# Kernel optimization log

Measured on AMD Instinct MI355X. Metric: run time of the kernel, lower is better.

The kernel has to match this reference:

```python
import jax, jax.numpy as jnp
import numpy as np

C_Z = 128
C_HID = 128

def setup_inputs() -> dict:
    key = jax.random.key(0)
    ks = jax.random.split(key, 8)
    B, N = 1, 512
    z = jax.random.normal(ks[0], (B, N, N, C_Z), dtype=jnp.float32)
    mask = jnp.ones((B, N, N), dtype=jnp.float32)
    s = 0.02
    params = {
        'ln_w': jnp.ones((C_Z,), jnp.float32),
        'ln_b': jnp.zeros((C_Z,), jnp.float32),
        'W_ap': jax.random.normal(ks[1], (C_Z, C_HID), jnp.float32) * s,
        'b_ap': jnp.zeros((C_HID,), jnp.float32),
        'W_ag': jax.random.normal(ks[2], (C_Z, C_HID), jnp.float32) * s,
        'b_ag': jnp.zeros((C_HID,), jnp.float32),
        'W_bp': jax.random.normal(ks[3], (C_Z, C_HID), jnp.float32) * s,
        'b_bp': jnp.zeros((C_HID,), jnp.float32),
        'W_bg': jax.random.normal(ks[4], (C_Z, C_HID), jnp.float32) * s,
        'b_bg': jnp.zeros((C_HID,), jnp.float32),
        'W_z': jax.random.normal(ks[5], (C_HID, C_Z), jnp.float32) * s,
        'b_z': jnp.zeros((C_Z,), jnp.float32),
    }
    return {'z': z, 'mask': mask, **params}

def _layer_norm(x, w, b, eps=1e-5):
    mu = jnp.mean(x, axis=-1, keepdims=True)
    var = jnp.mean(jnp.square(x - mu), axis=-1, keepdims=True)
    return (x - mu) * jax.lax.rsqrt(var + eps) * w + b

def reference(z, mask, ln_w, ln_b, W_ap, b_ap, W_ag, b_ag, W_bp, b_bp, W_bg, b_bg, W_z, b_z):
    # z: [B, N, N, c_z], mask: [B, N, N]
    z_norm = _layer_norm(z, ln_w, ln_b)
    m = mask[..., None]  # [B, N, N, 1]
    a = (z_norm @ W_ap + b_ap) * jax.nn.sigmoid(z_norm @ W_ag + b_ag) * m
    b = (z_norm @ W_bp + b_bp) * jax.nn.sigmoid(z_norm @ W_bg + b_bg) * m
    # outgoing triangle update: per-channel batched matmul over k
    out = jnp.einsum('bikc,bkjc->bijc', a, b)
    return z + (out @ W_z + b_z)
```

## Files before the change

kernel.cpp:

```cpp
#include <hip/hip_runtime.h>
#include <hip/hip_bf16.h>
#include <cstdint>

#define NN   512
#define CZ   128
#define PTOT (NN * NN)

typedef unsigned short u16;
typedef unsigned int   u32;

using f32x4  = __attribute__((ext_vector_type(4))) float;
using bf16x8 = __attribute__((ext_vector_type(8))) __bf16;

__device__ __forceinline__ u16 f2bf(float x) {
    u32 u = __float_as_uint(x);
    u = (u + 0x7fffu + ((u >> 16) & 1u)) >> 16;
    return (u16)u;
}

__device__ __forceinline__ f32x4 mfma16(bf16x8 a, bf16x8 b, f32x4 c) {
    return __builtin_amdgcn_mfma_f32_16x16x32_bf16(a, b, c, 0, 0, 0);
}

#define GLDS16(src, dst) __builtin_amdgcn_global_load_lds(                  \
        (__attribute__((address_space(1))) void*)(src),                     \
        (__attribute__((address_space(3))) void*)(dst), 16, 0, 0)

__global__ __launch_bounds__(256) void prep_w(
    const float* __restrict__ w0, const float* __restrict__ w1,
    const float* __restrict__ w2, const float* __restrict__ w3,
    const float* __restrict__ w4, u16* __restrict__ out)
{
    const float* srcs[5] = {w0, w1, w2, w3, w4};
    const float* src = srcs[blockIdx.x];
    u16* dst = out + blockIdx.x * 16384;
    for (int idx = threadIdx.x; idx < 16384; idx += 256) {
        int n = idx >> 7, k = idx & 127;
        dst[idx] = f2bf(src[k * 128 + n]);
    }
}

__global__ __launch_bounds__(256) void ln_k(
    const float* __restrict__ z, const float* __restrict__ lnw,
    const float* __restrict__ lnb, u16* __restrict__ zn)
{
    const int t = threadIdx.x;
    const int r = t >> 2, q = t & 3;
    const long prow = (long)blockIdx.x * 64 + r;
    const float4* zp = (const float4*)(z + prow * CZ + q * 32);

    float v[32];
    float s = 0.f, s2 = 0.f;
#pragma unroll
    for (int j = 0; j < 8; ++j) {
        float4 x = zp[j];
        v[j * 4 + 0] = x.x; v[j * 4 + 1] = x.y;
        v[j * 4 + 2] = x.z; v[j * 4 + 3] = x.w;
        s  += x.x + x.y + x.z + x.w;
        s2 += x.x * x.x + x.y * x.y + x.z * x.z + x.w * x.w;
    }
    s  += __shfl_xor(s, 1);  s  += __shfl_xor(s, 2);
    s2 += __shfl_xor(s2, 1); s2 += __shfl_xor(s2, 2);
    float mu  = s * (1.f / 128.f);
    float var = s2 * (1.f / 128.f) - mu * mu;
    float rs  = rsqrtf(var + 1e-5f);

    const float4* lwp = (const float4*)(lnw + q * 32);
    const float4* lbp = (const float4*)(lnb + q * 32);
    u32 pk[16];
#pragma unroll
    for (int j = 0; j < 8; ++j) {
        float4 lw = lwp[j], lb = lbp[j];
        float a0 = (v[j * 4 + 0] - mu) * rs * lw.x + lb.x;
        float a1 = (v[j * 4 + 1] - mu) * rs * lw.y + lb.y;
        float a2 = (v[j * 4 + 2] - mu) * rs * lw.z + lb.z;
        float a3 = (v[j * 4 + 3] - mu) * rs * lw.w + lb.w;
        pk[j * 2 + 0] = (u32)f2bf(a0) | ((u32)f2bf(a1) << 16);
        pk[j * 2 + 1] = (u32)f2bf(a2) | ((u32)f2bf(a3) << 16);
    }
    uint4* dst = (uint4*)(zn + prow * CZ + q * 32);
#pragma unroll
    for (int j = 0; j < 4; ++j) {
        uint4 w4; w4.x = pk[j*4]; w4.y = pk[j*4+1]; w4.z = pk[j*4+2]; w4.w = pk[j*4+3];
        dst[j] = w4;
    }
}

__global__ __launch_bounds__(256) void proj_k(
    const u16* __restrict__ zn,   const float* __restrict__ mask,
    const u16* __restrict__ Wt,
    const float* __restrict__ b_ap, const float* __restrict__ b_ag,
    const float* __restrict__ b_bp, const float* __restrict__ b_bg,
    u16* __restrict__ Aout, u16* __restrict__ Bout)
{
    __shared__ u16  znl[64 * 128];
    __shared__ u16  tbuf[128 * 72];
    __shared__ float lmask[64];

    const int t    = threadIdx.x, l = t & 63, w = t >> 6;
    const int tile = blockIdx.x;
    const int flav = blockIdx.y;
    const int ir   = tile >> 3;
    const int k0   = (tile & 7) << 6;

    {
        const int u = l & 15;
#pragma unroll
        for (int i = 0; i < 4; ++i) {
            int row = (w << 4) + (i << 2) + (l >> 4);
            long prow = flav ? ((long)(k0 + row) * NN + ir)
                             : ((long)ir * NN + k0 + row);
            const u16* src = zn + prow * CZ + ((u ^ (row & 15)) << 3);
            GLDS16(src, &znl[((w << 4) + (i << 2)) << 7]);
        }
    }
    if (t < 64) {
        long prow = flav ? ((long)(k0 + t) * NN + ir) : ((long)ir * NN + k0 + t);
        lmask[t] = mask[prow];
    }
    __syncthreads();

    const u16* Wp = Wt + (flav * 2 + 0) * 16384;
    const u16* Wg = Wt + (flav * 2 + 1) * 16384;

    f32x4 zero4 = {0.f, 0.f, 0.f, 0.f};
    f32x4 accP[4][2], accG[4][2];
#pragma unroll
    for (int mf = 0; mf < 4; ++mf)
#pragma unroll
        for (int nf = 0; nf < 2; ++nf) { accP[mf][nf] = zero4; accG[mf][nf] = zero4; }

#pragma unroll
    for (int kk = 0; kk < 4; ++kk) {
        bf16x8 af[4];
#pragma unroll
        for (int mf = 0; mf < 4; ++mf) {
            int row = (mf << 4) + (l & 15);
            int su  = (kk * 4 + (l >> 4)) ^ (row & 15);
            af[mf] = *(const bf16x8*)&znl[(row << 7) + (su << 3)];
        }
#pragma unroll
        for (int nf = 0; nf < 2; ++nf) {
            int n  = (w << 5) + (nf << 4) + (l & 15);
            int ko = (kk << 5) + ((l >> 4) << 3);
            bf16x8 bp = *(const bf16x8*)&Wp[(n << 7) + ko];
            bf16x8 bg = *(const bf16x8*)&Wg[(n << 7) + ko];
#pragma unroll
            for (int mf = 0; mf < 4; ++mf) {
                accP[mf][nf] = mfma16(af[mf], bp, accP[mf][nf]);
                accG[mf][nf] = mfma16(af[mf], bg, accG[mf][nf]);
            }
        }
    }

    const float* bPp = flav ? b_bp : b_ap;
    const float* bGp = flav ? b_bg : b_ag;
#pragma unroll
    for (int nf = 0; nf < 2; ++nf) {
        int col = (w << 5) + (nf << 4) + (l & 15);
        float bp = bPp[col], bg = bGp[col];
#pragma unroll
        for (int mf = 0; mf < 4; ++mf) {
            int row0 = (mf << 4) + ((l >> 4) << 2);
            float av[4];
#pragma unroll
            for (int rg = 0; rg < 4; ++rg) {
                float pv = accP[mf][nf][rg] + bp;
                float gv = accG[mf][nf][rg] + bg;
                av[rg] = pv * (1.f / (1.f + __expf(-gv))) * lmask[row0 + rg];
            }
            uint2 packed;
            packed.x = (u32)f2bf(av[0]) | ((u32)f2bf(av[1]) << 16);
            packed.y = (u32)f2bf(av[2]) | ((u32)f2bf(av[3]) << 16);
            *(uint2*)&tbuf[col * 72 + row0] = packed;
        }
    }
    __syncthreads();

    u16* outp = flav ? Bout : Aout;
    const int c = t >> 1, half = t & 1;
    u16* dst = outp + (size_t)c * PTOT + (size_t)ir * NN + k0 + half * 32;
    const u16* srcb = &tbuf[c * 72 + half * 32];
#pragma unroll
    for (int e = 0; e < 4; ++e)
        *(uint4*)(dst + e * 8) = *(const uint4*)(srcb + e * 8);
}

__global__ __launch_bounds__(256) void cgemm(
    const u16* __restrict__ A, const u16* __restrict__ B, u16* __restrict__ O)
{
    __shared__ u16 ldsA[2][128 * 64];
    __shared__ u16 ldsB[2][128 * 64];

    const int t = threadIdx.x, l = t & 63, w = t >> 6;
    const int bx0 = blockIdx.x;
    const int bx  = (bx0 & 7) * 256 + (bx0 >> 3);
    const int c  = bx >> 4, ti = (bx >> 2) & 3, tj = bx & 3;
    const u16* Ab = A + (size_t)c * PTOT + (size_t)(ti * 128) * NN;
    const u16* Bb = B + (size_t)c * PTOT + (size_t)(tj * 128) * NN;

    const int lr8 = (w << 3) + (l >> 3);
    const int uu  = l & 7;

    auto stage = [&](int buf, int kt) {
#pragma unroll
        for (int ri = 0; ri < 4; ++ri) {
            int row = ri * 32 + lr8;
            const u16* sa = Ab + (size_t)row * NN + (kt << 6) + ((uu ^ (row & 7)) << 3);
            const u16* sb = Bb + (size_t)row * NN + (kt << 6) + ((uu ^ (row & 7)) << 3);
            u16* da = &ldsA[buf][(ri * 32 + (w << 3)) << 6];
            u16* db = &ldsB[buf][(ri * 32 + (w << 3)) << 6];
            GLDS16(sa, da);
            GLDS16(sb, db);
        }
    };

    const int wm = w >> 1, wn = w & 1;
    f32x4 zero4 = {0.f, 0.f, 0.f, 0.f};
    f32x4 acc[4][4];
#pragma unroll
    for (int mf = 0; mf < 4; ++mf)
#pragma unroll
        for (int nf = 0; nf < 4; ++nf) acc[mf][nf] = zero4;

    stage(0, 0);
    __syncthreads();
    int cur = 0;
    for (int kt = 0; kt < 8; ++kt) {
        if (kt < 7) stage(cur ^ 1, kt + 1);
        const u16* lA = ldsA[cur];
        const u16* lB = ldsB[cur];
#pragma unroll
        for (int kk = 0; kk < 2; ++kk) {
            bf16x8 af[4], bfr[4];
#pragma unroll
            for (int mf = 0; mf < 4; ++mf) {
                int row = (wm << 6) + (mf << 4) + (l & 15);
                int su  = ((kk << 2) + (l >> 4)) ^ (row & 7);
                af[mf] = *(const bf16x8*)&lA[(row << 6) + (su << 3)];
            }
#pragma unroll
            for (int nf = 0; nf < 4; ++nf) {
                int row = (wn << 6) + (nf << 4) + (l & 15);
                int su  = ((kk << 2) + (l >> 4)) ^ (row & 7);
                bfr[nf] = *(const bf16x8*)&lB[(row << 6) + (su << 3)];
            }
#pragma unroll
            for (int mf = 0; mf < 4; ++mf)
#pragma unroll
                for (int nf = 0; nf < 4; ++nf)
                    acc[mf][nf] = mfma16(af[mf], bfr[nf], acc[mf][nf]);
        }
        if (kt < 7) __syncthreads();
        cur ^= 1;
    }

    u16* Ob = O + (size_t)c * PTOT;
    const int i0 = ti * 128 + (wm << 6);
    const int j0 = tj * 128 + (wn << 6);
#pragma unroll
    for (int mf = 0; mf < 4; ++mf)
#pragma unroll
        for (int nf = 0; nf < 4; ++nf) {
            int jc = j0 + (nf << 4) + (l & 15);
#pragma unroll
            for (int rg = 0; rg < 4; ++rg) {
                int irow = i0 + (mf << 4) + ((l >> 4) << 2) + rg;
                Ob[(size_t)irow * NN + jc] = f2bf(acc[mf][nf][rg]);
            }
        }
}

__global__ __launch_bounds__(256) void finalk(
    const u16* __restrict__ O, const u16* __restrict__ Wzt,
    const float* __restrict__ z, const float* __restrict__ bz,
    float* __restrict__ out)
{
    __shared__ u16 Ot[128 * 128];

    const int t = threadIdx.x, l = t & 63, w = t >> 6;
    const int p0 = blockIdx.x << 7;

#pragma unroll
    for (int rep = 0; rep < 8; ++rep) {
        int chunk = rep * 256 + t;
        int c  = chunk >> 4;
        int pc = chunk & 15;
        uint4 vv = *(const uint4*)(O + (size_t)c * PTOT + p0 + (pc << 3));
        const u16* vs = (const u16*)&vv;
#pragma unroll
        for (int e = 0; e < 8; ++e) {
            int p  = (pc << 3) + e;
            int su = (c >> 3) ^ ((p >> 3) & 15) ^ (p & 7);
            Ot[(p << 7) + (su << 3) + (c & 7)] = vs[e];
        }
    }
    __syncthreads();

    f32x4 zero4 = {0.f, 0.f, 0.f, 0.f};
    f32x4 acc[2][8];
#pragma unroll
    for (int mf = 0; mf < 2; ++mf)
#pragma unroll
        for (int nf = 0; nf < 8; ++nf) acc[mf][nf] = zero4;

#pragma unroll
    for (int kk = 0; kk < 4; ++kk) {
        bf16x8 af[2];
#pragma unroll
        for (int mf = 0; mf < 2; ++mf) {
            int p  = (w << 5) + (mf << 4) + (l & 15);
            int su = ((kk << 2) + (l >> 4)) ^ ((p >> 3) & 15) ^ (p & 7);
            af[mf] = *(const bf16x8*)&Ot[(p << 7) + (su << 3)];
        }
#pragma unroll
        for (int nf = 0; nf < 8; ++nf) {
            int co = (nf << 4) + (l & 15);
            bf16x8 bw = *(const bf16x8*)&Wzt[(co << 7) + (kk << 5) + ((l >> 4) << 3)];
#pragma unroll
            for (int mf = 0; mf < 2; ++mf)
                acc[mf][nf] = mfma16(af[mf], bw, acc[mf][nf]);
        }
    }

#pragma unroll
    for (int nf = 0; nf < 8; ++nf) {
        int co = (nf << 4) + (l & 15);
        float b = bz[co];
#pragma unroll
        for (int mf = 0; mf < 2; ++mf) {
#pragma unroll
            for (int rg = 0; rg < 4; ++rg) {
                int p = (w << 5) + (mf << 4) + ((l >> 4) << 2) + rg;
                size_t idx = (size_t)(p0 + p) * CZ + co;
                out[idx] = z[idx] + acc[mf][nf][rg] + b;
            }
        }
    }
}

extern "C" void kernel_launch(void* const* d_in, const int* in_sizes, int n_in,
                              void* d_out, int out_size, void* d_ws, size_t ws_size,
                              hipStream_t stream)
{
    const float* z    = (const float*)d_in[0];
    const float* mask = (const float*)d_in[1];
    const float* lnw  = (const float*)d_in[2];
    const float* lnb  = (const float*)d_in[3];
    const float* Wap  = (const float*)d_in[4];
    const float* bap  = (const float*)d_in[5];
    const float* Wag  = (const float*)d_in[6];
    const float* bag  = (const float*)d_in[7];
    const float* Wbp  = (const float*)d_in[8];
    const float* bbp  = (const float*)d_in[9];
    const float* Wbg  = (const float*)d_in[10];
    const float* bbg  = (const float*)d_in[11];
    const float* Wz   = (const float*)d_in[12];
    const float* bz   = (const float*)d_in[13];
    float* out = (float*)d_out;

    u16* A_t  = (u16*)d_ws;
    u16* B_tt = A_t  + (size_t)CZ * PTOT;
    u16* O_t  = B_tt + (size_t)CZ * PTOT;
    u16* Wt   = O_t  + (size_t)CZ * PTOT;
    u16* Wzt  = Wt + 4 * 16384;
    u16* zn   = O_t;

    prep_w<<<5, 256, 0, stream>>>(Wap, Wag, Wbp, Wbg, Wz, Wt);
    ln_k<<<4096, 256, 0, stream>>>(z, lnw, lnb, zn);
    proj_k<<<dim3(4096, 2), 256, 0, stream>>>(zn, mask, Wt,
                                              bap, bag, bbp, bbg, A_t, B_tt);
    cgemm<<<2048, 256, 0, stream>>>(A_t, B_tt, O_t);
    finalk<<<2048, 256, 0, stream>>>(O_t, Wzt, z, bz, out);
}
```

Measured before the change: 600.9 us.

## Vectorize finalk transpose into LDS and swap MFMA operands for float4 epilogue

The final projection kernel now loads eight channel rows per thread and packs them into 16-byte LDS stores with a new swizzle, replacing scalar 2-byte LDS writes. The MFMA operands are swapped so the weights form the A operand and positions the B operand. Each lane then holds four consecutive output channels, so the residual read of z and the output write become float4 accesses instead of scalar ones. This targets LDS store count and uncoalesced global traffic in the epilogue, at the cost of more registers for the eight held loads.

```diff
diff --git a/kernel.cpp b/kernel.cpp
--- a/kernel.cpp
+++ b/kernel.cpp
@@ -281,60 +281,74 @@
     const int t = threadIdx.x, l = t & 63, w = t >> 6;
     const int p0 = blockIdx.x << 7;
 
-#pragma unroll
-    for (int rep = 0; rep < 8; ++rep) {
-        int chunk = rep * 256 + t;
-        int c  = chunk >> 4;
-        int pc = chunk & 15;
-        uint4 vv = *(const uint4*)(O + (size_t)c * PTOT + p0 + (pc << 3));
-        const u16* vs = (const u16*)&vv;
+    {
+        const int po = t & 15;
+        const int uc = t >> 4;
+        uint4 q[8];
+#pragma unroll
+        for (int cc = 0; cc < 8; ++cc)
+            q[cc] = *(const uint4*)(O + (size_t)(uc * 8 + cc) * PTOT + p0 + po * 8);
 #pragma unroll
         for (int e = 0; e < 8; ++e) {
-            int p  = (pc << 3) + e;
-            int su = (c >> 3) ^ ((p >> 3) & 15) ^ (p & 7);
-            Ot[(p << 7) + (su << 3) + (c & 7)] = vs[e];
+            const int sh = (e & 1) * 16;
+            const int wd = e >> 1;
+            u32 h[8];
+#pragma unroll
+            for (int cc = 0; cc < 8; ++cc)
+                h[cc] = (((const u32*)&q[cc])[wd] >> sh) & 0xffffu;
+            uint4 o;
+            o.x = h[0] | (h[1] << 16);
+            o.y = h[2] | (h[3] << 16);
+            o.z = h[4] | (h[5] << 16);
+            o.w = h[6] | (h[7] << 16);
+            int p  = po * 8 + e;
+            int su = uc ^ (p & 15) ^ ((p >> 4) & 7);
+            *(uint4*)&Ot[(p << 7) + (su << 3)] = o;
         }
     }
     __syncthreads();
 
     f32x4 zero4 = {0.f, 0.f, 0.f, 0.f};
-    f32x4 acc[2][8];
-#pragma unroll
-    for (int mf = 0; mf < 2; ++mf)
-#pragma unroll
-        for (int nf = 0; nf < 8; ++nf) acc[mf][nf] = zero4;
+    f32x4 acc[8][2];
+#pragma unroll
+    for (int m = 0; m < 8; ++m)
+#pragma unroll
+        for (int np = 0; np < 2; ++np) acc[m][np] = zero4;
 
 #pragma unroll
     for (int kk = 0; kk < 4; ++kk) {
-        bf16x8 af[2];
-#pragma unroll
-        for (int mf = 0; mf < 2; ++mf) {
-            int p  = (w << 5) + (mf << 4) + (l & 15);
-            int su = ((kk << 2) + (l >> 4)) ^ ((p >> 3) & 15) ^ (p & 7);
-            af[mf] = *(const bf16x8*)&Ot[(p << 7) + (su << 3)];
-        }
-#pragma unroll
-        for (int nf = 0; nf < 8; ++nf) {
-            int co = (nf << 4) + (l & 15);
-            bf16x8 bw = *(const bf16x8*)&Wzt[(co << 7) + (kk << 5) + ((l >> 4) << 3)];
-#pragma unroll
-            for (int mf = 0; mf < 2; ++mf)
-                acc[mf][nf] = mfma16(af[mf], bw, acc[mf][nf]);
-        }
-    }
-
-#pragma unroll
-    for (int nf = 0; nf < 8; ++nf) {
-        int co = (nf << 4) + (l & 15);
-        float b = bz[co];
-#pragma unroll
-        for (int mf = 0; mf < 2; ++mf) {
-#pragma unroll
-            for (int rg = 0; rg < 4; ++rg) {
-                int p = (w << 5) + (mf << 4) + ((l >> 4) << 2) + rg;
-                size_t idx = (size_t)(p0 + p) * CZ + co;
-                out[idx] = z[idx] + acc[mf][nf][rg] + b;
-            }
+        bf16x8 af[8];
+#pragma unroll
+        for (int m = 0; m < 8; ++m) {
+            int co = (m << 4) + (l & 15);
+            af[m] = *(const bf16x8*)&Wzt[(co << 7) + (kk << 5) + ((l >> 4) << 3)];
+        }
+#pragma unroll
+        for (int np = 0; np < 2; ++np) {
+            int p  = (w << 5) + (np << 4) + (l & 15);
+            int su = ((kk << 2) + (l >> 4)) ^ (p & 15) ^ ((p >> 4) & 7);
+            bf16x8 bfr = *(const bf16x8*)&Ot[(p << 7) + (su << 3)];
+#pragma unroll
+            for (int m = 0; m < 8; ++m)
+                acc[m][np] = mfma16(af[m], bfr, acc[m][np]);
+        }
+    }
+
+#pragma unroll
+    for (int m = 0; m < 8; ++m) {
+        const int co4 = (m << 4) + ((l >> 4) << 2);
+        const float4 bv = *(const float4*)&bz[co4];
+#pragma unroll
+        for (int np = 0; np < 2; ++np) {
+            int p = p0 + (w << 5) + (np << 4) + (l & 15);
+            size_t idx = (size_t)p * CZ + co4;
+            float4 zv = *(const float4*)&z[idx];
+            float4 ov;
+            ov.x = zv.x + acc[m][np][0] + bv.x;
+            ov.y = zv.y + acc[m][np][1] + bv.y;
+            ov.z = zv.z + acc[m][np][2] + bv.z;
+            ov.w = zv.w + acc[m][np][3] + bv.w;
+            *(float4*)&out[idx] = ov;
         }
     }
 }
```

Result: faster. 536.8 us (-10.7%).
